# Performance work log

Measured on AMD Instinct MI355X. Metric: run time of the kernel, lower is better.

The kernel has to match this reference:

```python
import jax, jax.numpy as jnp
import numpy as np

D_MODEL = 512
N_HEADS = 8
HEAD_DIM = 64
INNER = N_HEADS * HEAD_DIM
PAD = 128  # flash-attention style tile padding used by the custom kernel


def setup_inputs() -> dict:
    key = jax.random.key(0)
    ks = jax.random.split(key, 5)
    B, S = 2, 2048
    scale = 0.02
    return {
        "hidden_states": jax.random.normal(ks[0], (B, S, D_MODEL), dtype=jnp.float32),
        "Wq": jax.random.normal(ks[1], (D_MODEL, INNER), dtype=jnp.float32) * scale,
        "Wk": jax.random.normal(ks[2], (D_MODEL, INNER), dtype=jnp.float32) * scale,
        "Wv": jax.random.normal(ks[3], (D_MODEL, INNER), dtype=jnp.float32) * scale,
        "Wo": jax.random.normal(ks[4], (INNER, D_MODEL), dtype=jnp.float32) * scale,
    }


def _padded_attention(q, k, v):
    """Emulates torch.ops.knl.fwd: pad seq to a multiple of PAD, run
    non-causal scaled dot-product attention masking padded keys, then
    slice back to the original length. q,k,v: [B, S, INNER]."""
    B, S, _ = q.shape
    pad_len = (-S) % PAD
    Sp = S + pad_len
    pad_cfg = ((0, 0), (0, pad_len), (0, 0))
    qp = jnp.pad(q, pad_cfg)
    kp = jnp.pad(k, pad_cfg)
    vp = jnp.pad(v, pad_cfg)
    # [B, H, Sp, hd]
    qh = qp.reshape(B, Sp, N_HEADS, HEAD_DIM).transpose(0, 2, 1, 3)
    kh = kp.reshape(B, Sp, N_HEADS, HEAD_DIM).transpose(0, 2, 1, 3)
    vh = vp.reshape(B, Sp, N_HEADS, HEAD_DIM).transpose(0, 2, 1, 3)
    scale = 1.0 / np.sqrt(HEAD_DIM).astype(np.float32)
    scores = jnp.einsum("bhqd,bhkd->bhqk", qh, kh) * scale  # [B,H,Sp,Sp]
    key_valid = jnp.arange(Sp) < S  # mask out padded keys
    scores = jnp.where(key_valid[None, None, None, :], scores, jnp.float32(-1e30))
    probs = jax.nn.softmax(scores, axis=-1)
    out = jnp.einsum("bhqk,bhkd->bhqd", probs, vh)  # [B,H,Sp,hd]
    out = out.transpose(0, 2, 1, 3).reshape(B, Sp, INNER)
    return out[:, :S, :]


def reference(hidden_states, Wq, Wk, Wv, Wo):
    q = hidden_states @ Wq
    k = hidden_states @ Wk
    v = hidden_states @ Wv
    attn = _padded_attention(q, k, v)
    return attn @ Wo
```

## Files before the change

### kernel.cpp

```cpp
#include <hip/hip_runtime.h>

using bf16 = __bf16;
using bf16x4 = __attribute__((ext_vector_type(4))) __bf16;
using bf16x8 = __attribute__((ext_vector_type(8))) __bf16;
using floatx4 = __attribute__((ext_vector_type(4))) float;
using half4 = __attribute__((ext_vector_type(4))) _Float16;
using half8 = __attribute__((ext_vector_type(8))) _Float16;

#define D_MODEL 512
#define S_LEN 2048
#define HD 64
#define NH 8
#define M_TOT 4096
#define NSPLIT 4
#define KSPAN (S_LEN / NSPLIT)
#define QSCALE 0.18033688f

__device__ __forceinline__ bf16x8 ld8(const bf16* p) {
    return *reinterpret_cast<const bf16x8*>(p);
}
__device__ __forceinline__ void gl_lds16(const bf16* g, bf16* l) {
    __builtin_amdgcn_global_load_lds(
        (const __attribute__((address_space(1))) void*)g,
        (__attribute__((address_space(3))) void*)l, 16, 0, 0);
}

__global__ __launch_bounds__(256) void prep(const float* __restrict__ w0,
                                            const float* __restrict__ w1,
                                            const float* __restrict__ w2,
                                            const float* __restrict__ w3,
                                            const float* __restrict__ X,
                                            bf16* __restrict__ WT,
                                            bf16* __restrict__ Xb) {
    int z = blockIdx.z;
    if (z == 4) {
        int i = (blockIdx.x * 256 + threadIdx.x) * 8;
        float4 a = *reinterpret_cast<const float4*>(X + i);
        float4 b = *reinterpret_cast<const float4*>(X + i + 4);
        bf16x8 o;
        o[0] = (bf16)a.x; o[1] = (bf16)a.y; o[2] = (bf16)a.z; o[3] = (bf16)a.w;
        o[4] = (bf16)b.x; o[5] = (bf16)b.y; o[6] = (bf16)b.z; o[7] = (bf16)b.w;
        *reinterpret_cast<bf16x8*>(Xb + i) = o;
        return;
    }
    if (blockIdx.x >= 256) return;
    __shared__ float t[32][33];
    const float* in = z == 0 ? w0 : z == 1 ? w1 : z == 2 ? w2 : w3;
    bf16* o = WT + (size_t)z * D_MODEL * D_MODEL;
    int x = threadIdx.x & 31;
    int y = threadIdx.x >> 5;
    int k0 = (blockIdx.x & 15) * 32, n0 = (blockIdx.x >> 4) * 32;
    for (int r = y; r < 32; r += 8) t[r][x] = in[(size_t)(k0 + r) * D_MODEL + n0 + x];
    __syncthreads();
    for (int r = y; r < 32; r += 8) o[(size_t)(n0 + r) * D_MODEL + k0 + x] = (bf16)t[x][r];
}

__global__ __launch_bounds__(256) void gemm_qkvf(const bf16* __restrict__ X,
                                                 const bf16* __restrict__ WT,
                                                 bf16* __restrict__ qk,
                                                 bf16* __restrict__ VT) {
    __shared__ __align__(16) bf16 As[64 * 64];
    __shared__ __align__(16) bf16 Bs[64 * 64];
    int lane = threadIdx.x & 63, wave = threadIdx.x >> 6;
    int l15 = lane & 15, quad = lane >> 4;
    int m0 = blockIdx.x * 64;
    int n0 = blockIdx.y * 64;
    int z = n0 >> 9;
    int h = (n0 >> 6) & 7;
    int wm = (wave & 1) * 32, wn = (wave >> 1) * 32;
    float oscale = (z == 0) ? QSCALE : 1.0f;

    int sr = lane >> 3;
    int sc = (lane & 7) ^ sr;
    const bf16* gA = X  + (size_t)(m0 + wave * 16 + sr) * D_MODEL + sc * 8;
    const bf16* gB = WT + (size_t)(n0 + wave * 16 + sr) * D_MODEL + sc * 8;
    bf16* ldsA = &As[(wave * 16) * 64];
    bf16* ldsB = &Bs[(wave * 16) * 64];
    int rx = l15 & 7;

    floatx4 acc[2][2] = {};
    for (int k0 = 0; k0 < D_MODEL; k0 += 64) {
        __syncthreads();
        gl_lds16(gA + k0, ldsA);
        gl_lds16(gA + (size_t)8 * D_MODEL + k0, ldsA + 8 * 64);
        gl_lds16(gB + k0, ldsB);
        gl_lds16(gB + (size_t)8 * D_MODEL + k0, ldsB + 8 * 64);
        __syncthreads();
        bf16x8 af[2][2], bfr[2][2];
        #pragma unroll
        for (int mt = 0; mt < 2; mt++)
            #pragma unroll
            for (int kh = 0; kh < 2; kh++)
                af[mt][kh] = ld8(&As[(wm + mt * 16 + l15) * 64 + (((quad + 4 * kh) ^ rx)) * 8]);
        #pragma unroll
        for (int nt = 0; nt < 2; nt++)
            #pragma unroll
            for (int kh = 0; kh < 2; kh++)
                bfr[nt][kh] = ld8(&Bs[(wn + nt * 16 + l15) * 64 + (((quad + 4 * kh) ^ rx)) * 8]);
        #pragma unroll
        for (int mt = 0; mt < 2; mt++)
            #pragma unroll
            for (int nt = 0; nt < 2; nt++) {
                acc[mt][nt] = __builtin_amdgcn_mfma_f32_16x16x32_bf16(af[mt][0], bfr[nt][0], acc[mt][nt], 0, 0, 0);
                acc[mt][nt] = __builtin_amdgcn_mfma_f32_16x16x32_bf16(af[mt][1], bfr[nt][1], acc[mt][nt], 0, 0, 0);
            }
    }

    if (z < 2) {
        bf16* dst = qk + (size_t)z * M_TOT * HD * NH;
        #pragma unroll
        for (int mt = 0; mt < 2; mt++)
            #pragma unroll
            for (int nt = 0; nt < 2; nt++)
                #pragma unroll
                for (int r = 0; r < 4; r++) {
                    int m = m0 + wm + mt * 16 + quad * 4 + r;
                    int n = wn + nt * 16 + l15;
                    int b = m >> 11, s = m & 2047;
                    dst[((size_t)(b * NH + h) * S_LEN + s) * HD + n] = (bf16)(acc[mt][nt][r] * oscale);
                }
    } else {
        #pragma unroll
        for (int mt = 0; mt < 2; mt++)
            #pragma unroll
            for (int nt = 0; nt < 2; nt++) {
                int m = m0 + wm + mt * 16 + quad * 4;
                int d = wn + nt * 16 + l15;
                int b = m >> 11, s = m & 2047;
                bf16x4 pk;
                pk[0] = (bf16)acc[mt][nt][0]; pk[1] = (bf16)acc[mt][nt][1];
                pk[2] = (bf16)acc[mt][nt][2]; pk[3] = (bf16)acc[mt][nt][3];
                *reinterpret_cast<bf16x4*>(&VT[((size_t)(b * NH + h) * HD + d) * S_LEN + s]) = pk;
            }
    }
}

__global__ __launch_bounds__(256, 8) void attn_split(const bf16* __restrict__ qg,
                                                     const bf16* __restrict__ kg,
                                                     const bf16* __restrict__ vt,
                                                     _Float16* __restrict__ Opart,
                                                     float* __restrict__ lsum) {
    __shared__ __align__(16) bf16 Kl[64 * 64];
    __shared__ __align__(16) bf16 Vl[64 * 64];
    int tid = threadIdx.x;
    int lane = tid & 63, wave = tid >> 6;
    int l15 = lane & 15, quad = lane >> 4;
    int bh = blockIdx.y, split = blockIdx.z;
    int q0 = blockIdx.x * 64;
    const bf16* qb = qg + (size_t)bh * S_LEN * HD;
    const bf16* kb = kg + (size_t)bh * S_LEN * HD + (size_t)split * KSPAN * HD;
    const bf16* vb = vt + (size_t)bh * HD * S_LEN + split * KSPAN;
    int q = q0 + wave * 16 + l15;
    bf16x8 qf0 = ld8(qb + (size_t)q * HD + quad * 8);
    bf16x8 qf1 = ld8(qb + (size_t)q * HD + 32 + quad * 8);
    floatx4 O[4] = {};
    float l_i = 0.f;

    int sr = lane >> 3;
    int sc = (lane & 7) ^ sr;
    const bf16* gK = kb + (size_t)(wave * 16 + sr) * HD + sc * 8;
    const bf16* gV = vb + (size_t)(wave * 16 + sr) * S_LEN + sc * 8;
    bf16* ldsK = &Kl[(wave * 16) * 64];
    bf16* ldsV = &Vl[(wave * 16) * 64];
    int rx = l15 & 7;
    int sa = ((quad & 1) << 5) + l15;
    int sb = sa + 16;
    bool himux = (quad & 2) != 0;

    for (int kt = 0; kt < KSPAN; kt += 64) {
        __syncthreads();
        gl_lds16(gK + (size_t)kt * HD, ldsK);
        gl_lds16(gK + (size_t)(kt + 8) * HD, ldsK + 8 * 64);
        gl_lds16(gV + kt, ldsV);
        gl_lds16(gV + (size_t)8 * S_LEN + kt, ldsV + 8 * 64);
        __syncthreads();

        floatx4 sc4[4];
        #pragma unroll
        for (int nt = 0; nt < 4; nt++) {
            floatx4 z = {};
            bf16x8 a0 = ld8(&Kl[(nt * 16 + l15) * 64 + (quad ^ rx) * 8]);
            bf16x8 a1 = ld8(&Kl[(nt * 16 + l15) * 64 + ((quad + 4) ^ rx) * 8]);
            z = __builtin_amdgcn_mfma_f32_16x16x32_bf16(a0, qf0, z, 0, 0, 0);
            z = __builtin_amdgcn_mfma_f32_16x16x32_bf16(a1, qf1, z, 0, 0, 0);
            sc4[nt] = z;
        }

        int2 pq[4];
        #pragma unroll
        for (int nt = 0; nt < 4; nt++) {
            bf16x4 pk;
            #pragma unroll
            for (int r = 0; r < 4; r++) {
                float p = exp2f(sc4[nt][r]);
                l_i += p;
                pk[r] = (bf16)p;
            }
            pq[nt] = __builtin_bit_cast(int2, pk);
        }

        bf16x8 pb[2];
        #pragma unroll
        for (int h2 = 0; h2 < 2; h2++) {
            int t0 = __shfl(pq[2 * h2].x,     sa, 64);
            int t1 = __shfl(pq[2 * h2].y,     sa, 64);
            int t2 = __shfl(pq[2 * h2 + 1].x, sa, 64);
            int t3 = __shfl(pq[2 * h2 + 1].y, sa, 64);
            int u0 = __shfl(pq[2 * h2].x,     sb, 64);
            int u1 = __shfl(pq[2 * h2].y,     sb, 64);
            int u2 = __shfl(pq[2 * h2 + 1].x, sb, 64);
            int u3 = __shfl(pq[2 * h2 + 1].y, sb, 64);
            int4 v;
            v.x = himux ? t2 : t0;
            v.y = himux ? t3 : t1;
            v.z = himux ? u2 : u0;
            v.w = himux ? u3 : u1;
            pb[h2] = __builtin_bit_cast(bf16x8, v);
        }

        #pragma unroll
        for (int nt = 0; nt < 4; nt++) {
            bf16x8 v0 = ld8(&Vl[(nt * 16 + l15) * 64 + (quad ^ rx) * 8]);
            bf16x8 v1 = ld8(&Vl[(nt * 16 + l15) * 64 + ((quad + 4) ^ rx) * 8]);
            O[nt] = __builtin_amdgcn_mfma_f32_16x16x32_bf16(v0, pb[0], O[nt], 0, 0, 0);
            O[nt] = __builtin_amdgcn_mfma_f32_16x16x32_bf16(v1, pb[1], O[nt], 0, 0, 0);
        }
    }

    l_i += __shfl_xor(l_i, 16, 64);
    l_i += __shfl_xor(l_i, 32, 64);

    size_t obase = (((size_t)(split * 16 + bh)) * S_LEN + q) * HD;
    #pragma unroll
    for (int nt = 0; nt < 4; nt++) {
        half4 hv;
        hv[0] = (_Float16)O[nt][0]; hv[1] = (_Float16)O[nt][1];
        hv[2] = (_Float16)O[nt][2]; hv[3] = (_Float16)O[nt][3];
        *reinterpret_cast<half4*>(&Opart[obase + nt * 16 + quad * 4]) = hv;
    }
    if (quad == 0)
        lsum[((size_t)(split * 16 + bh)) * S_LEN + q] = l_i;
}

__global__ __launch_bounds__(256) void gemm_outm(const _Float16* __restrict__ Opart,
                                                 const float* __restrict__ lsum,
                                                 const bf16* __restrict__ WoT,
                                                 float* __restrict__ out) {
    __shared__ __align__(16) bf16 As[64 * 64];
    __shared__ __align__(16) bf16 Bs[64 * 64];
    __shared__ float invl[64 * 8];
    int tid = threadIdx.x;
    int lane = tid & 63, wave = tid >> 6;
    int l15 = lane & 15, quad = lane >> 4;
    int m0 = blockIdx.x * 64;
    int n0 = blockIdx.y * 64;
    int wm = (wave & 1) * 32, wn = (wave >> 1) * 32;

    for (int i = tid; i < 512; i += 256) {
        int row = i >> 3, h = i & 7;
        int mm = m0 + row;
        int b = mm >> 11, q = mm & 2047;
        float l = 0.f;
        #pragma unroll
        for (int s = 0; s < NSPLIT; s++)
            l += lsum[((size_t)(s * 16 + b * NH + h)) * S_LEN + q];
        invl[i] = 1.f / l;
    }

    int sr = lane >> 3;
    int sc = (lane & 7) ^ sr;
    const bf16* gB = WoT + (size_t)(n0 + wave * 16 + sr) * D_MODEL + sc * 8;
    bf16* ldsA = &As[(wave * 16) * 64];
    bf16* ldsB = &Bs[(wave * 16) * 64];
    int rx = l15 & 7;

    floatx4 acc[2][2] = {};
    for (int k0 = 0; k0 < D_MODEL; k0 += 64) {
        __syncthreads();
        gl_lds16(gB + k0, ldsB);
        gl_lds16(gB + (size_t)8 * D_MODEL + k0, ldsB + 8 * 64);
        int h = k0 >> 6;
        #pragma unroll
        for (int st = 0; st < 2; st++) {
            int row = wave * 16 + sr + st * 8;
            int mm = m0 + row;
            int b = mm >> 11, q = mm & 2047;
            float iv = invl[row * 8 + h];
            float a8[8] = {};
            #pragma unroll
            for (int s = 0; s < NSPLIT; s++) {
                half8 hp = *reinterpret_cast<const half8*>(
                    &Opart[(((size_t)(s * 16 + b * NH + h)) * S_LEN + q) * HD + sc * 8]);
                #pragma unroll
                for (int j = 0; j < 8; j++) a8[j] += (float)hp[j];
            }
            bf16x8 v;
            #pragma unroll
            for (int j = 0; j < 8; j++) v[j] = (bf16)(a8[j] * iv);
            *reinterpret_cast<bf16x8*>(ldsA + st * 512 + lane * 8) = v;
        }
        __syncthreads();
        bf16x8 af[2][2], bfr[2][2];
        #pragma unroll
        for (int mt = 0; mt < 2; mt++)
            #pragma unroll
            for (int kh = 0; kh < 2; kh++)
                af[mt][kh] = ld8(&As[(wm + mt * 16 + l15) * 64 + (((quad + 4 * kh) ^ rx)) * 8]);
        #pragma unroll
        for (int nt = 0; nt < 2; nt++)
            #pragma unroll
            for (int kh = 0; kh < 2; kh++)
                bfr[nt][kh] = ld8(&Bs[(wn + nt * 16 + l15) * 64 + (((quad + 4 * kh) ^ rx)) * 8]);
        #pragma unroll
        for (int mt = 0; mt < 2; mt++)
            #pragma unroll
            for (int nt = 0; nt < 2; nt++) {
                acc[mt][nt] = __builtin_amdgcn_mfma_f32_16x16x32_bf16(af[mt][0], bfr[nt][0], acc[mt][nt], 0, 0, 0);
                acc[mt][nt] = __builtin_amdgcn_mfma_f32_16x16x32_bf16(af[mt][1], bfr[nt][1], acc[mt][nt], 0, 0, 0);
            }
    }

    #pragma unroll
    for (int mt = 0; mt < 2; mt++)
        #pragma unroll
        for (int nt = 0; nt < 2; nt++)
            #pragma unroll
            for (int r = 0; r < 4; r++) {
                int m = m0 + wm + mt * 16 + quad * 4 + r;
                int n = n0 + wn + nt * 16 + l15;
                out[(size_t)m * D_MODEL + n] = acc[mt][nt][r];
            }
}

extern "C" void kernel_launch(void* const* d_in, const int* in_sizes, int n_in,
                              void* d_out, int out_size, void* d_ws, size_t ws_size,
                              hipStream_t stream) {
    const float* X  = (const float*)d_in[0];
    const float* Wq = (const float*)d_in[1];
    const float* Wk = (const float*)d_in[2];
    const float* Wv = (const float*)d_in[3];
    const float* Wo = (const float*)d_in[4];
    float* out = (float*)d_out;
    bf16* ws  = (bf16*)d_ws;

    bf16* Xb  = ws;
    bf16* WT  = Xb + (size_t)M_TOT * D_MODEL;
    bf16* qk  = WT + (size_t)4 * D_MODEL * D_MODEL;
    bf16* VT  = qk + (size_t)2 * M_TOT * D_MODEL;
    _Float16* Opart = (_Float16*)(VT + (size_t)M_TOT * D_MODEL);
    float* lbuf = (float*)(Opart + (size_t)NSPLIT * 16 * S_LEN * HD);

    prep<<<dim3(1024, 1, 5), 256, 0, stream>>>(Wq, Wk, Wv, Wo, X, WT, Xb);
    gemm_qkvf<<<dim3(64, 24), 256, 0, stream>>>(Xb, WT, qk, VT);
    attn_split<<<dim3(32, 16, NSPLIT), 256, 0, stream>>>(qk,
                                                         qk + (size_t)M_TOT * D_MODEL,
                                                         VT, Opart, lbuf);
    gemm_outm<<<dim3(64, 8), 256, 0, stream>>>(Opart, lbuf,
                                               WT + (size_t)3 * D_MODEL * D_MODEL, out);
}
```

Measured before the change: 130.7 us.

## Double-buffer K/V LDS tiles in split attention kernel

Gives the K and V shared-memory tiles two buffers. The loads for the next key tile are issued right after the barrier and land while the current tile is being computed. This removes one barrier per iteration and hides global-to-LDS load latency behind the QK, softmax and PV work. In exchange it doubles LDS use per block to 32KB, which may cut the number of resident blocks per CU below the declared 8.

```diff
diff --git a/kernel.cpp b/kernel.cpp
--- a/kernel.cpp
+++ b/kernel.cpp
@@ -14,6 +14,7 @@
 #define M_TOT 4096
 #define NSPLIT 4
 #define KSPAN (S_LEN / NSPLIT)
+#define NT_TILES (KSPAN / 64)
 #define QSCALE 0.18033688f
 
 __device__ __forceinline__ bf16x8 ld8(const bf16* p) {
@@ -140,8 +141,8 @@
                                                      const bf16* __restrict__ vt,
                                                      _Float16* __restrict__ Opart,
                                                      float* __restrict__ lsum) {
-    __shared__ __align__(16) bf16 Kl[64 * 64];
-    __shared__ __align__(16) bf16 Vl[64 * 64];
+    __shared__ __align__(16) bf16 Kl[2][64 * 64];
+    __shared__ __align__(16) bf16 Vl[2][64 * 64];
     int tid = threadIdx.x;
     int lane = tid & 63, wave = tid >> 6;
     int l15 = lane & 15, quad = lane >> 4;
@@ -160,27 +161,37 @@
     int sc = (lane & 7) ^ sr;
     const bf16* gK = kb + (size_t)(wave * 16 + sr) * HD + sc * 8;
     const bf16* gV = vb + (size_t)(wave * 16 + sr) * S_LEN + sc * 8;
-    bf16* ldsK = &Kl[(wave * 16) * 64];
-    bf16* ldsV = &Vl[(wave * 16) * 64];
+    int ldsOff = (wave * 16) * 64;
     int rx = l15 & 7;
     int sa = ((quad & 1) << 5) + l15;
     int sb = sa + 16;
     bool himux = (quad & 2) != 0;
 
-    for (int kt = 0; kt < KSPAN; kt += 64) {
-        __syncthreads();
-        gl_lds16(gK + (size_t)kt * HD, ldsK);
-        gl_lds16(gK + (size_t)(kt + 8) * HD, ldsK + 8 * 64);
-        gl_lds16(gV + kt, ldsV);
-        gl_lds16(gV + (size_t)8 * S_LEN + kt, ldsV + 8 * 64);
-        __syncthreads();
+    gl_lds16(gK, &Kl[0][ldsOff]);
+    gl_lds16(gK + (size_t)8 * HD, &Kl[0][ldsOff + 8 * 64]);
+    gl_lds16(gV, &Vl[0][ldsOff]);
+    gl_lds16(gV + (size_t)8 * S_LEN, &Vl[0][ldsOff + 8 * 64]);
+
+    for (int t = 0; t < NT_TILES; t++) {
+        int bsel = t & 1;
+        __syncthreads();
+        if (t + 1 < NT_TILES) {
+            int kt = (t + 1) * 64;
+            int nb = bsel ^ 1;
+            gl_lds16(gK + (size_t)kt * HD, &Kl[nb][ldsOff]);
+            gl_lds16(gK + (size_t)(kt + 8) * HD, &Kl[nb][ldsOff + 8 * 64]);
+            gl_lds16(gV + kt, &Vl[nb][ldsOff]);
+            gl_lds16(gV + (size_t)8 * S_LEN + kt, &Vl[nb][ldsOff + 8 * 64]);
+        }
+        const bf16* Kb = Kl[bsel];
+        const bf16* Vb = Vl[bsel];
 
         floatx4 sc4[4];
         #pragma unroll
         for (int nt = 0; nt < 4; nt++) {
             floatx4 z = {};
-            bf16x8 a0 = ld8(&Kl[(nt * 16 + l15) * 64 + (quad ^ rx) * 8]);
-            bf16x8 a1 = ld8(&Kl[(nt * 16 + l15) * 64 + ((quad + 4) ^ rx) * 8]);
+            bf16x8 a0 = ld8(&Kb[(nt * 16 + l15) * 64 + (quad ^ rx) * 8]);
+            bf16x8 a1 = ld8(&Kb[(nt * 16 + l15) * 64 + ((quad + 4) ^ rx) * 8]);
             z = __builtin_amdgcn_mfma_f32_16x16x32_bf16(a0, qf0, z, 0, 0, 0);
             z = __builtin_amdgcn_mfma_f32_16x16x32_bf16(a1, qf1, z, 0, 0, 0);
             sc4[nt] = z;
@@ -220,8 +231,8 @@
 
         #pragma unroll
         for (int nt = 0; nt < 4; nt++) {
-            bf16x8 v0 = ld8(&Vl[(nt * 16 + l15) * 64 + (quad ^ rx) * 8]);
-            bf16x8 v1 = ld8(&Vl[(nt * 16 + l15) * 64 + ((quad + 4) ^ rx) * 8]);
+            bf16x8 v0 = ld8(&Vb[(nt * 16 + l15) * 64 + (quad ^ rx) * 8]);
+            bf16x8 v1 = ld8(&Vb[(nt * 16 + l15) * 64 + ((quad + 4) ^ rx) * 8]);
             O[nt] = __builtin_amdgcn_mfma_f32_16x16x32_bf16(v0, pb[0], O[nt], 0, 0, 0);
             O[nt] = __builtin_amdgcn_mfma_f32_16x16x32_bf16(v1, pb[1], O[nt], 0, 0, 0);
         }
```

After: 134.2 us. 2.7% more time.
